# Kernel optimization log

Hardware: AMD Instinct MI355X
Metric: run time of the kernel (lower is better)

Reference implementation:

```python
import jax, jax.numpy as jnp
import numpy as np

N_NODES = 100000
N_EDGES = 1600000
S_FEAT = 16   # static node features
D_FEAT = 8    # dynamic node features
E_FEAT = 4    # edge features
K = 2
EDGE_IN = E_FEAT + 2 * S_FEAT + 2 * D_FEAT  # 52
HIDDEN = 2 * D_FEAT                          # 16


def setup_inputs() -> dict:
    key = jax.random.key(0)
    ks = jax.random.split(key, 12)
    inp = {
        "x_s": jax.random.normal(ks[0], (N_NODES, S_FEAT), jnp.float32),
        "x_d": jax.random.normal(ks[1], (N_NODES, D_FEAT), jnp.float32),
        "edge_attr": jax.random.normal(ks[2], (N_EDGES, E_FEAT), jnp.float32),
        # edge MLP: Linear(EDGE_IN->HIDDEN) + ReLU + Linear(HIDDEN->D_FEAT)
        "W1": jax.random.normal(ks[3], (HIDDEN, EDGE_IN), jnp.float32) / np.sqrt(EDGE_IN),
        "b1": jnp.zeros((HIDDEN,), jnp.float32),
        "W2": jax.random.normal(ks[4], (D_FEAT, HIDDEN), jnp.float32) / np.sqrt(HIDDEN),
        "b2": jnp.zeros((D_FEAT,), jnp.float32),
        # K+1 = 3 filter matrices, Linear(D->D, bias=False): y = x @ W.T
        "Wf0": jax.random.normal(ks[5], (D_FEAT, D_FEAT), jnp.float32) / np.sqrt(D_FEAT),
        "Wf1": jax.random.normal(ks[6], (D_FEAT, D_FEAT), jnp.float32) / np.sqrt(D_FEAT),
        "Wf2": jax.random.normal(ks[7], (D_FEAT, D_FEAT), jnp.float32) / np.sqrt(D_FEAT),
        "edge_index": jax.random.randint(ks[8], (2, N_EDGES), 0, N_NODES, jnp.int64
                                         if jax.config.jax_enable_x64 else jnp.int32),
    }
    return inp


def _edge_mlp(e, W1, b1, W2, b2):
    h = jax.nn.relu(e @ W1.T + b1)
    return h @ W2.T + b2


def reference(x_s, x_d, edge_attr, W1, b1, W2, b2, Wf0, Wf1, Wf2, edge_index):
    row, col = edge_index[0], edge_index[1]
    num_nodes = x_d.shape[0]

    # s_ij depends only on static inputs (x_s, x_d, edge_attr), not on `out`,
    # so it is identical across the K steps; compute it once. The per-step
    # boolean edge mask is applied multiplicatively below, which matches the
    # torch masked-gather/scatter exactly (normalization is per-edge).
    e_ij = jnp.concatenate(
        [x_s[row], x_s[col], x_d[row], x_d[col], edge_attr], axis=1)  # [E, 52]
    s_ij = _edge_mlp(e_ij, W1, b1, W2, b2)                            # [E, D]
    nrm = jnp.linalg.norm(s_ij, axis=1, keepdims=True)
    s_ij = jnp.where(nrm > 0, s_ij / jnp.where(nrm > 0, nrm, 1.0), 0.0)

    filters = [Wf0, Wf1, Wf2]
    out = x_d @ filters[0].T
    for k in range(K):
        mask = out.sum(1) != 0                         # [N]
        edge_mask = (mask[row] | mask[col]).astype(out.dtype)  # [E]
        hydraulic_gradient = out[col] - out[row]       # [E, D]
        shift_sum = hydraulic_gradient * s_ij * edge_mask[:, None]
        scattered = jax.ops.segment_sum(shift_sum, col, num_segments=num_nodes)
        scattered = scattered @ filters[k + 1].T
        out = out + scattered
    return out
```

## Files before the change

kernel.cpp:

```cpp
#include <hip/hip_runtime.h>
#include <hip/hip_fp16.h>

#define S_FEAT 16
#define D_FEAT 8
#define E_FEAT 4
#define EDGE_IN 52
#define HIDDEN 16
#define SCAN_CHUNK 2048
#define NSUB 8

typedef unsigned int uint4v __attribute__((ext_vector_type(4)));
typedef float float4v __attribute__((ext_vector_type(4)));
typedef int int2v __attribute__((ext_vector_type(2)));

__device__ __forceinline__ void mlp_sij(
    const float* __restrict__ x_s, const float* __restrict__ x_d,
    const float* __restrict__ edge_attr,
    const float* __restrict__ W1, const float* __restrict__ b1,
    const float* __restrict__ W2, const float* __restrict__ b2,
    int row, int col, int e, float s[D_FEAT])
{
    float in[EDGE_IN];
    {
        const float4* p = (const float4*)(x_s + (size_t)row * S_FEAT);
#pragma unroll
        for (int q = 0; q < 4; ++q) {
            float4 v = p[q];
            in[q * 4 + 0] = v.x; in[q * 4 + 1] = v.y;
            in[q * 4 + 2] = v.z; in[q * 4 + 3] = v.w;
        }
    }
    {
        const float4* p = (const float4*)(x_s + (size_t)col * S_FEAT);
#pragma unroll
        for (int q = 0; q < 4; ++q) {
            float4 v = p[q];
            in[16 + q * 4 + 0] = v.x; in[16 + q * 4 + 1] = v.y;
            in[16 + q * 4 + 2] = v.z; in[16 + q * 4 + 3] = v.w;
        }
    }
    {
        const float4* p = (const float4*)(x_d + (size_t)row * D_FEAT);
#pragma unroll
        for (int q = 0; q < 2; ++q) {
            float4 v = p[q];
            in[32 + q * 4 + 0] = v.x; in[32 + q * 4 + 1] = v.y;
            in[32 + q * 4 + 2] = v.z; in[32 + q * 4 + 3] = v.w;
        }
    }
    {
        const float4* p = (const float4*)(x_d + (size_t)col * D_FEAT);
#pragma unroll
        for (int q = 0; q < 2; ++q) {
            float4 v = p[q];
            in[40 + q * 4 + 0] = v.x; in[40 + q * 4 + 1] = v.y;
            in[40 + q * 4 + 2] = v.z; in[40 + q * 4 + 3] = v.w;
        }
    }
    {
        float4 v = *(const float4*)(edge_attr + (size_t)e * E_FEAT);
        in[48] = v.x; in[49] = v.y; in[50] = v.z; in[51] = v.w;
    }

    float h[HIDDEN];
#pragma unroll
    for (int i = 0; i < HIDDEN; ++i) {
        float acc = b1[i];
#pragma unroll
        for (int j = 0; j < EDGE_IN; ++j)
            acc = fmaf(in[j], W1[i * EDGE_IN + j], acc);
        h[i] = acc > 0.f ? acc : 0.f;
    }

    float nrm2 = 0.f;
#pragma unroll
    for (int i = 0; i < D_FEAT; ++i) {
        float acc = b2[i];
#pragma unroll
        for (int j = 0; j < HIDDEN; ++j)
            acc = fmaf(h[j], W2[i * HIDDEN + j], acc);
        s[i] = acc;
        nrm2 = fmaf(acc, acc, nrm2);
    }
    float nrm = sqrtf(nrm2);
    float inv = nrm > 0.f ? 1.f / nrm : 0.f;
#pragma unroll
    for (int i = 0; i < D_FEAT; ++i) s[i] *= inv;
}

__device__ __forceinline__ uint4v pack_rec(const float s[8], int row)
{
    int q[8];
#pragma unroll
    for (int i = 0; i < 8; ++i) {
        float v = fminf(fmaxf(s[i] * 2047.f, -2047.f), 2047.f);
        q[i] = (int)rintf(v) & 0xFFF;
    }
    uint4v r;
    r[0] = (unsigned)(q[0] | (q[1] << 12) | (q[2] << 24));
    r[1] = (unsigned)((q[2] >> 8) | (q[3] << 4) | (q[4] << 16) | (q[5] << 28));
    r[2] = (unsigned)((q[5] >> 4) | (q[6] << 8) | (q[7] << 20));
    r[3] = (unsigned)row;
    return r;
}

__device__ __forceinline__ float rec_s(uint4v r, int f)
{
    int off = f * 12;
    unsigned lo = off < 32 ? r[0] : (off < 64 ? r[1] : r[2]);
    unsigned hi = off < 32 ? r[1] : (off < 64 ? r[2] : 0u);
    unsigned sh = (unsigned)off & 31u;
    unsigned long long both = ((unsigned long long)hi << 32) | lo;
    int q = ((int)((unsigned)(both >> sh) << 20)) >> 20;
    return (float)q * (1.f / 2047.f);
}

__device__ __forceinline__ void unpack8h(uint4v w, float* dst)
{
#pragma unroll
    for (int i = 0; i < 4; ++i) {
        unsigned u = w[i];
        __half2 h = *reinterpret_cast<__half2*>(&u);
        float2 f = __half22float2(h);
        dst[2 * i] = f.x; dst[2 * i + 1] = f.y;
    }
}

__global__ __launch_bounds__(256) void zero_counts_kernel(int* __restrict__ counts, int M)
{
    int i = blockIdx.x * blockDim.x + threadIdx.x;
    if (i < M) counts[i] = 0;
}

__global__ __launch_bounds__(256) void hist_kernel(
    const int* __restrict__ ei, int E, int N, int* __restrict__ counts8)
{
    int e = blockIdx.x * blockDim.x + threadIdx.x;
    if (e >= E) return;
    int col = __builtin_nontemporal_load(ei + E + e);
    atomicAdd(&counts8[(threadIdx.x & (NSUB - 1)) * N + col], 1);
}

__global__ __launch_bounds__(256) void scan_local_kernel(
    const int* __restrict__ counts8, int* __restrict__ partial,
    int* __restrict__ blocksums, int N)
{
    __shared__ int sh[256];
    int b = blockIdx.x, t = threadIdx.x;
    int base = b * SCAN_CHUNK + t * 8;
    int v[8];
    int run = 0;
#pragma unroll
    for (int j = 0; j < 8; ++j) {
        int c = 0;
        if (base + j < N) {
#pragma unroll
            for (int s8 = 0; s8 < NSUB; ++s8)
                c += counts8[s8 * N + base + j];
        }
        v[j] = run;
        run += c;
    }
    sh[t] = run;
    __syncthreads();
#pragma unroll
    for (int st = 1; st < 256; st <<= 1) {
        int x = (t >= st) ? sh[t - st] : 0;
        __syncthreads();
        sh[t] += x;
        __syncthreads();
    }
    int excl = sh[t] - run;
    if (t == 255) blocksums[b] = sh[255];
#pragma unroll
    for (int j = 0; j < 8; ++j)
        if (base + j < N) partial[base + j] = excl + v[j];
}

__global__ __launch_bounds__(64) void scan_blk_kernel(int* __restrict__ bs, int NB)
{
    int lane = threadIdx.x;
    int carry = 0;
    for (int base = 0; base < NB; base += 64) {
        int i = base + lane;
        int orig = (i < NB) ? bs[i] : 0;
        int v = orig;
#pragma unroll
        for (int st = 1; st < 64; st <<= 1) {
            int t = __shfl_up(v, st);
            if (lane >= st) v += t;
        }
        if (i < NB) bs[i] = carry + v - orig;
        carry += __shfl(v, 63);
    }
}

__global__ __launch_bounds__(256) void scan_add_kernel(
    int* __restrict__ offsets, int* __restrict__ cursor,
    const int* __restrict__ blocksums, int N, int E)
{
    int i = blockIdx.x * blockDim.x + threadIdx.x;
    if (i < N) {
        int off = offsets[i] + blocksums[i / SCAN_CHUNK];
        offsets[i] = off;
        cursor[i]  = off;
    } else if (i == N) {
        offsets[N] = E;
    }
}

__global__ __launch_bounds__(256) void proj_scan_kernel(
    int* __restrict__ offsets, int* __restrict__ cursor,
    const int* __restrict__ blocksums,
    const float* __restrict__ x_s, const float* __restrict__ x_d,
    const float* __restrict__ W1, const float* __restrict__ b1,
    const float* __restrict__ Wf0,
    __half* __restrict__ PRh, __half* __restrict__ PCh,
    float* __restrict__ out, int N, int E)
{
    int n = blockIdx.x * blockDim.x + threadIdx.x;
    if (n > N) return;
    if (n == N) { offsets[N] = E; return; }
    {
        int off = offsets[n] + blocksums[n / SCAN_CHUNK];
        offsets[n] = off;
        cursor[n]  = off;
    }
    float xs[S_FEAT], xd[D_FEAT];
    {
        const float4* p = (const float4*)(x_s + (size_t)n * S_FEAT);
#pragma unroll
        for (int q = 0; q < 4; ++q) {
            float4 v = p[q];
            xs[q * 4 + 0] = v.x; xs[q * 4 + 1] = v.y;
            xs[q * 4 + 2] = v.z; xs[q * 4 + 3] = v.w;
        }
        const float4* pd = (const float4*)(x_d + (size_t)n * D_FEAT);
        float4 a = pd[0], b = pd[1];
        xd[0] = a.x; xd[1] = a.y; xd[2] = a.z; xd[3] = a.w;
        xd[4] = b.x; xd[5] = b.y; xd[6] = b.z; xd[7] = b.w;
    }
    __half prh[HIDDEN], pch[HIDDEN];
#pragma unroll
    for (int i = 0; i < HIDDEN; ++i) {
        const float* w = W1 + i * EDGE_IN;
        float a = b1[i], c = 0.f;
#pragma unroll
        for (int j = 0; j < S_FEAT; ++j) {
            a = fmaf(xs[j], w[j], a);
            c = fmaf(xs[j], w[16 + j], c);
        }
#pragma unroll
        for (int j = 0; j < D_FEAT; ++j) {
            a = fmaf(xd[j], w[32 + j], a);
            c = fmaf(xd[j], w[40 + j], c);
        }
        prh[i] = __float2half_rn(a);
        pch[i] = __float2half_rn(c);
    }
    {
        uint4v* pr = (uint4v*)(PRh + (size_t)n * HIDDEN);
        uint4v* pc = (uint4v*)(PCh + (size_t)n * HIDDEN);
        pr[0] = *(uint4v*)&prh[0]; pr[1] = *(uint4v*)&prh[8];
        pc[0] = *(uint4v*)&pch[0]; pc[1] = *(uint4v*)&pch[8];
    }
    float o[D_FEAT];
#pragma unroll
    for (int i = 0; i < D_FEAT; ++i) {
        float acc = 0.f;
#pragma unroll
        for (int j = 0; j < D_FEAT; ++j)
            acc = fmaf(xd[j], Wf0[i * D_FEAT + j], acc);
        o[i] = acc;
    }
    float4* op = (float4*)(out + (size_t)n * D_FEAT);
    op[0] = make_float4(o[0], o[1], o[2], o[3]);
    op[1] = make_float4(o[4], o[5], o[6], o[7]);
}

__device__ __forceinline__ void edge_work(
    const __half* __restrict__ PRh, const __half* __restrict__ PCh,
    const float* __restrict__ edge_attr,
    const float* __restrict__ W1,
    const float* __restrict__ W2, const float* __restrict__ b2,
    int row, int col, int e,
    int* __restrict__ cursor, uint4v* __restrict__ recs)
{
    float pr[HIDDEN], pc[HIDDEN];
    {
        const uint4v* p = (const uint4v*)(PRh + (size_t)row * HIDDEN);
        const uint4v* c = (const uint4v*)(PCh + (size_t)col * HIDDEN);
        uint4v p0 = p[0], p1 = p[1], c0 = c[0], c1 = c[1];
        unpack8h(p0, pr); unpack8h(p1, pr + 8);
        unpack8h(c0, pc); unpack8h(c1, pc + 8);
    }
    float4v ea = __builtin_nontemporal_load(
        (const float4v*)(edge_attr + (size_t)e * E_FEAT));

    float h[HIDDEN];
#pragma unroll
    for (int i = 0; i < HIDDEN; ++i) {
        const float* w = W1 + i * EDGE_IN + 48;
        float acc = pr[i] + pc[i];
        acc = fmaf(ea[0], w[0], acc);
        acc = fmaf(ea[1], w[1], acc);
        acc = fmaf(ea[2], w[2], acc);
        acc = fmaf(ea[3], w[3], acc);
        h[i] = acc > 0.f ? acc : 0.f;
    }

    float s[D_FEAT];
    float nrm2 = 0.f;
#pragma unroll
    for (int i = 0; i < D_FEAT; ++i) {
        float acc = b2[i];
#pragma unroll
        for (int j = 0; j < HIDDEN; ++j)
            acc = fmaf(h[j], W2[i * HIDDEN + j], acc);
        s[i] = acc;
        nrm2 = fmaf(acc, acc, nrm2);
    }
    float nrm = sqrtf(nrm2);
    float inv = nrm > 0.f ? 1.f / nrm : 0.f;
#pragma unroll
    for (int i = 0; i < D_FEAT; ++i) s[i] *= inv;

    uint4v rec = pack_rec(s, row);
    int pos = atomicAdd(&cursor[col], 1);
    __builtin_nontemporal_store(rec, recs + pos);
}

__global__ __launch_bounds__(256) void mlp_scatter_proj_kernel(
    const __half* __restrict__ PRh, const __half* __restrict__ PCh,
    const float* __restrict__ edge_attr,
    const float* __restrict__ W1,
    const float* __restrict__ W2, const float* __restrict__ b2,
    const int* __restrict__ ei, int E,
    int* __restrict__ cursor, uint4v* __restrict__ recs)
{
    int e0 = (blockIdx.x * blockDim.x + threadIdx.x) * 2;
    if (e0 >= E) return;
    if (e0 + 1 < E) {
        int2v rows = __builtin_nontemporal_load((const int2v*)(ei + e0));
        int2v cols = __builtin_nontemporal_load((const int2v*)(ei + E + e0));
        edge_work(PRh, PCh, edge_attr, W1, W2, b2, rows[0], cols[0], e0,     cursor, recs);
        edge_work(PRh, PCh, edge_attr, W1, W2, b2, rows[1], cols[1], e0 + 1, cursor, recs);
    } else {
        int row = ei[e0], col = ei[E + e0];
        edge_work(PRh, PCh, edge_attr, W1, W2, b2, row, col, e0, cursor, recs);
    }
}

__global__ __launch_bounds__(256) void mlp_scatter_direct_kernel(
    const float* __restrict__ x_s, const float* __restrict__ x_d,
    const float* __restrict__ edge_attr,
    const float* __restrict__ W1, const float* __restrict__ b1,
    const float* __restrict__ W2, const float* __restrict__ b2,
    const int* __restrict__ ei, int E,
    int* __restrict__ cursor, uint4v* __restrict__ recs)
{
    int e = blockIdx.x * blockDim.x + threadIdx.x;
    if (e >= E) return;
    int row = ei[e], col = ei[E + e];
    float s[D_FEAT];
    mlp_sij(x_s, x_d, edge_attr, W1, b1, W2, b2, row, col, e, s);
    uint4v rec = pack_rec(s, row);
    int pos = atomicAdd(&cursor[col], 1);
    __builtin_nontemporal_store(rec, recs + pos);
}

__global__ __launch_bounds__(256) void node_init_kernel(
    const float* __restrict__ x_d, const float* __restrict__ Wf0,
    float* __restrict__ out, int N)
{
    int n = blockIdx.x * blockDim.x + threadIdx.x;
    if (n >= N) return;
    float xd[D_FEAT];
    const float4* p = (const float4*)(x_d + (size_t)n * D_FEAT);
    float4 a = p[0], b = p[1];
    xd[0] = a.x; xd[1] = a.y; xd[2] = a.z; xd[3] = a.w;
    xd[4] = b.x; xd[5] = b.y; xd[6] = b.z; xd[7] = b.w;
    float o[D_FEAT];
#pragma unroll
    for (int i = 0; i < D_FEAT; ++i) {
        float acc = 0.f;
#pragma unroll
        for (int j = 0; j < D_FEAT; ++j)
            acc = fmaf(xd[j], Wf0[i * D_FEAT + j], acc);
        o[i] = acc;
    }
    float4* op = (float4*)(out + (size_t)n * D_FEAT);
    op[0] = make_float4(o[0], o[1], o[2], o[3]);
    op[1] = make_float4(o[4], o[5], o[6], o[7]);
}

__global__ __launch_bounds__(256) void csr_step_kernel(
    const float* __restrict__ out_in, float* __restrict__ out_out,
    const int* __restrict__ offsets, const uint4v* __restrict__ recs,
    const float* __restrict__ Wf, int N)
{
    int lane = threadIdx.x & 63;
    int node = blockIdx.x * 4 + (threadIdx.x >> 6);
    if (node >= N) return;
    int e_sub = lane >> 3, f = lane & 7;
    int beg = offsets[node], end = offsets[node + 1];
    float outc = out_in[(size_t)node * 8 + f];
    float sc = outc;
    sc += __shfl_xor(sc, 1); sc += __shfl_xor(sc, 2); sc += __shfl_xor(sc, 4);
    bool mc = (sc != 0.f);
    float acc = 0.f;
    for (int base = beg; base < end; base += 8) {
        int e = base + e_sub;
        bool valid = e < end;
        uint4v rec = (uint4v)(0u);
        if (valid) rec = __builtin_nontemporal_load(recs + e);
        int row = (int)rec[3];
        float s = rec_s(rec, f);
        float outr = out_in[(size_t)row * 8 + f];
        float sr = outr;
        sr += __shfl_xor(sr, 1); sr += __shfl_xor(sr, 2); sr += __shfl_xor(sr, 4);
        acc += (mc || sr != 0.f) ? (outc - outr) * s : 0.f;
    }
    acc += __shfl_xor(acc, 8);
    acc += __shfl_xor(acc, 16);
    acc += __shfl_xor(acc, 32);
    float upd = 0.f;
#pragma unroll
    for (int j = 0; j < 8; ++j) {
        float aj = __shfl(acc, (lane & ~7) | j);
        upd = fmaf(Wf[f * 8 + j], aj, upd);
    }
    if (e_sub == 0)
        out_out[(size_t)node * 8 + f] = outc + upd;
}

__global__ __launch_bounds__(256) void fb_node_init_kernel(
    const float* __restrict__ x_d, const float* __restrict__ Wf0,
    float* __restrict__ out, float* __restrict__ scattered, int N)
{
    int n = blockIdx.x * blockDim.x + threadIdx.x;
    if (n >= N) return;
    float xd[D_FEAT];
    const float4* p = (const float4*)(x_d + (size_t)n * D_FEAT);
    float4 a = p[0], b = p[1];
    xd[0] = a.x; xd[1] = a.y; xd[2] = a.z; xd[3] = a.w;
    xd[4] = b.x; xd[5] = b.y; xd[6] = b.z; xd[7] = b.w;
    float o[D_FEAT];
#pragma unroll
    for (int i = 0; i < D_FEAT; ++i) {
        float acc = 0.f;
#pragma unroll
        for (int j = 0; j < D_FEAT; ++j)
            acc = fmaf(xd[j], Wf0[i * D_FEAT + j], acc);
        o[i] = acc;
    }
    float4* op = (float4*)(out + (size_t)n * D_FEAT);
    op[0] = make_float4(o[0], o[1], o[2], o[3]);
    op[1] = make_float4(o[4], o[5], o[6], o[7]);
    float4* sp = (float4*)(scattered + (size_t)n * D_FEAT);
    sp[0] = make_float4(0.f, 0.f, 0.f, 0.f);
    sp[1] = make_float4(0.f, 0.f, 0.f, 0.f);
}

__global__ __launch_bounds__(256) void fb_edge_step_kernel(
    const float* __restrict__ x_s, const float* __restrict__ x_d,
    const float* __restrict__ edge_attr,
    const float* __restrict__ W1, const float* __restrict__ b1,
    const float* __restrict__ W2, const float* __restrict__ b2,
    const float* __restrict__ out,
    const int* __restrict__ ei, int E, float* __restrict__ scattered)
{
    int e = blockIdx.x * blockDim.x + threadIdx.x;
    if (e >= E) return;
    int row = ei[e], col = ei[E + e];
    const float4* pr = (const float4*)(out + (size_t)row * D_FEAT);
    const float4* pc = (const float4*)(out + (size_t)col * D_FEAT);
    float4 r0 = pr[0], r1 = pr[1], c0 = pc[0], c1 = pc[1];
    float srow = r0.x + r0.y + r0.z + r0.w + r1.x + r1.y + r1.z + r1.w;
    float scol = c0.x + c0.y + c0.z + c0.w + c1.x + c1.y + c1.z + c1.w;
    if (srow == 0.f && scol == 0.f) return;
    float s[D_FEAT];
    mlp_sij(x_s, x_d, edge_attr, W1, b1, W2, b2, row, col, e, s);
    float* dst = scattered + (size_t)col * D_FEAT;
    atomicAdd(dst + 0, (c0.x - r0.x) * s[0]);
    atomicAdd(dst + 1, (c0.y - r0.y) * s[1]);
    atomicAdd(dst + 2, (c0.z - r0.z) * s[2]);
    atomicAdd(dst + 3, (c0.w - r0.w) * s[3]);
    atomicAdd(dst + 4, (c1.x - r1.x) * s[4]);
    atomicAdd(dst + 5, (c1.y - r1.y) * s[5]);
    atomicAdd(dst + 6, (c1.z - r1.z) * s[6]);
    atomicAdd(dst + 7, (c1.w - r1.w) * s[7]);
}

__global__ __launch_bounds__(256) void fb_node_update_kernel(
    float* __restrict__ out, float* __restrict__ scattered,
    const float* __restrict__ Wf, int N)
{
    int n = blockIdx.x * blockDim.x + threadIdx.x;
    if (n >= N) return;
    float sc[D_FEAT];
    float4* sp = (float4*)(scattered + (size_t)n * D_FEAT);
    float4 a = sp[0], b = sp[1];
    sc[0] = a.x; sc[1] = a.y; sc[2] = a.z; sc[3] = a.w;
    sc[4] = b.x; sc[5] = b.y; sc[6] = b.z; sc[7] = b.w;
    sp[0] = make_float4(0.f, 0.f, 0.f, 0.f);
    sp[1] = make_float4(0.f, 0.f, 0.f, 0.f);
    float4* op = (float4*)(out + (size_t)n * D_FEAT);
    float4 o0 = op[0], o1 = op[1];
    float o[D_FEAT] = {o0.x, o0.y, o0.z, o0.w, o1.x, o1.y, o1.z, o1.w};
#pragma unroll
    for (int i = 0; i < D_FEAT; ++i) {
        float acc = 0.f;
#pragma unroll
        for (int j = 0; j < D_FEAT; ++j)
            acc = fmaf(sc[j], Wf[i * D_FEAT + j], acc);
        o[i] += acc;
    }
    op[0] = make_float4(o[0], o[1], o[2], o[3]);
    op[1] = make_float4(o[4], o[5], o[6], o[7]);
}

extern "C" void kernel_launch(void* const* d_in, const int* in_sizes, int n_in,
                              void* d_out, int out_size, void* d_ws, size_t ws_size,
                              hipStream_t stream) {
    const float* x_s       = (const float*)d_in[0];
    const float* x_d       = (const float*)d_in[1];
    const float* edge_attr = (const float*)d_in[2];
    const float* W1        = (const float*)d_in[3];
    const float* b1        = (const float*)d_in[4];
    const float* W2        = (const float*)d_in[5];
    const float* b2        = (const float*)d_in[6];
    const float* Wf[3]     = {(const float*)d_in[7], (const float*)d_in[8],
                              (const float*)d_in[9]};
    const int*   ei        = (const int*)d_in[10];

    const int N = in_sizes[1] / D_FEAT;
    const int E = in_sizes[10] / 2;

    float* out = (float*)d_out;

    size_t off = 0;
    auto carve = [&](size_t bytes) { size_t p = off; off = (off + bytes + 255) & ~255ULL; return p; };
    size_t o_counts  = carve((size_t)NSUB * N * 4);
    size_t o_offsets = carve((size_t)(N + 1) * 4);
    size_t o_cursor  = carve((size_t)(N + 1) * 4);
    size_t o_bsums   = carve(256 * 4);
    size_t o_bufA    = carve((size_t)N * D_FEAT * 4);
    size_t o_recs    = carve((size_t)E * 16);
    const size_t need_base = off;
    size_t o_PR      = carve((size_t)N * HIDDEN * 2);
    size_t o_PC      = carve((size_t)N * HIDDEN * 2);
    const size_t need_full = off;

    dim3 blk(256);
    dim3 gE((E + 255) / 256);
    dim3 gN((N + 255) / 256);

    if (ws_size >= need_base) {
        char* ws = (char*)d_ws;
        int*   counts8 = (int*)(ws + o_counts);
        int*   offsets = (int*)(ws + o_offsets);
        int*   cursor  = (int*)(ws + o_cursor);
        int*   bsums   = (int*)(ws + o_bsums);
        float* bufA    = (float*)(ws + o_bufA);
        uint4v* recs   = (uint4v*)(ws + o_recs);

        const int NB = (N + SCAN_CHUNK - 1) / SCAN_CHUNK;

        zero_counts_kernel<<<dim3((NSUB * N + 255) / 256), blk, 0, stream>>>(counts8, NSUB * N);
        hist_kernel<<<gE, blk, 0, stream>>>(ei, E, N, counts8);
        scan_local_kernel<<<dim3(NB), blk, 0, stream>>>(counts8, offsets, bsums, N);
        scan_blk_kernel<<<dim3(1), dim3(64), 0, stream>>>(bsums, NB);

        if (ws_size >= need_full) {
            __half* PRh = (__half*)(ws + o_PR);
            __half* PCh = (__half*)(ws + o_PC);
            proj_scan_kernel<<<dim3((N + 256) / 256), blk, 0, stream>>>(
                offsets, cursor, bsums, x_s, x_d, W1, b1, Wf[0],
                PRh, PCh, out, N, E);
            mlp_scatter_proj_kernel<<<dim3((E / 2 + 255) / 256), blk, 0, stream>>>(
                PRh, PCh, edge_attr, W1, W2, b2, ei, E, cursor, recs);
        } else {
            scan_add_kernel<<<dim3((N + 256) / 256), blk, 0, stream>>>(offsets, cursor, bsums, N, E);
            node_init_kernel<<<gN, blk, 0, stream>>>(x_d, Wf[0], out, N);
            mlp_scatter_direct_kernel<<<gE, blk, 0, stream>>>(
                x_s, x_d, edge_attr, W1, b1, W2, b2, ei, E, cursor, recs);
        }

        dim3 gC((N + 3) / 4);
        csr_step_kernel<<<gC, blk, 0, stream>>>(out, bufA, offsets, recs, Wf[1], N);
        csr_step_kernel<<<gC, blk, 0, stream>>>(bufA, out, offsets, recs, Wf[2], N);
    } else {
        float* scattered = (float*)d_ws;
        fb_node_init_kernel<<<gN, blk, 0, stream>>>(x_d, Wf[0], out, scattered, N);
        for (int k = 0; k < 2; ++k) {
            fb_edge_step_kernel<<<gE, blk, 0, stream>>>(
                x_s, x_d, edge_attr, W1, b1, W2, b2, out, ei, E, scattered);
            fb_node_update_kernel<<<gN, blk, 0, stream>>>(out, scattered, Wf[k + 1], N);
        }
    }
}
```

Baseline: 375.3 us.

## Fold block-sum scan into last scan block and replace zero kernel with memset

Removes the separate single-block scan kernel by having the last-finishing scan_local block, detected via an atomic done counter, perform the block-sum prefix scan. The zero-count kernel becomes a hipMemsetAsync that also clears the done counter. The edge MLP kernel now handles one edge per thread instead of two. This cuts launch count and serialization, at the cost of threadfence/atomic traffic and possibly less per-thread ILP in the edge kernel.

```diff
diff --git a/kernel.cpp b/kernel.cpp
--- a/kernel.cpp
+++ b/kernel.cpp
@@ -11,82 +11,6 @@
 
 typedef unsigned int uint4v __attribute__((ext_vector_type(4)));
 typedef float float4v __attribute__((ext_vector_type(4)));
-typedef int int2v __attribute__((ext_vector_type(2)));
-
-__device__ __forceinline__ void mlp_sij(
-    const float* __restrict__ x_s, const float* __restrict__ x_d,
-    const float* __restrict__ edge_attr,
-    const float* __restrict__ W1, const float* __restrict__ b1,
-    const float* __restrict__ W2, const float* __restrict__ b2,
-    int row, int col, int e, float s[D_FEAT])
-{
-    float in[EDGE_IN];
-    {
-        const float4* p = (const float4*)(x_s + (size_t)row * S_FEAT);
-#pragma unroll
-        for (int q = 0; q < 4; ++q) {
-            float4 v = p[q];
-            in[q * 4 + 0] = v.x; in[q * 4 + 1] = v.y;
-            in[q * 4 + 2] = v.z; in[q * 4 + 3] = v.w;
-        }
-    }
-    {
-        const float4* p = (const float4*)(x_s + (size_t)col * S_FEAT);
-#pragma unroll
-        for (int q = 0; q < 4; ++q) {
-            float4 v = p[q];
-            in[16 + q * 4 + 0] = v.x; in[16 + q * 4 + 1] = v.y;
-            in[16 + q * 4 + 2] = v.z; in[16 + q * 4 + 3] = v.w;
-        }
-    }
-    {
-        const float4* p = (const float4*)(x_d + (size_t)row * D_FEAT);
-#pragma unroll
-        for (int q = 0; q < 2; ++q) {
-            float4 v = p[q];
-            in[32 + q * 4 + 0] = v.x; in[32 + q * 4 + 1] = v.y;
-            in[32 + q * 4 + 2] = v.z; in[32 + q * 4 + 3] = v.w;
-        }
-    }
-    {
-        const float4* p = (const float4*)(x_d + (size_t)col * D_FEAT);
-#pragma unroll
-        for (int q = 0; q < 2; ++q) {
-            float4 v = p[q];
-            in[40 + q * 4 + 0] = v.x; in[40 + q * 4 + 1] = v.y;
-            in[40 + q * 4 + 2] = v.z; in[40 + q * 4 + 3] = v.w;
-        }
-    }
-    {
-        float4 v = *(const float4*)(edge_attr + (size_t)e * E_FEAT);
-        in[48] = v.x; in[49] = v.y; in[50] = v.z; in[51] = v.w;
-    }
-
-    float h[HIDDEN];
-#pragma unroll
-    for (int i = 0; i < HIDDEN; ++i) {
-        float acc = b1[i];
-#pragma unroll
-        for (int j = 0; j < EDGE_IN; ++j)
-            acc = fmaf(in[j], W1[i * EDGE_IN + j], acc);
-        h[i] = acc > 0.f ? acc : 0.f;
-    }
-
-    float nrm2 = 0.f;
-#pragma unroll
-    for (int i = 0; i < D_FEAT; ++i) {
-        float acc = b2[i];
-#pragma unroll
-        for (int j = 0; j < HIDDEN; ++j)
-            acc = fmaf(h[j], W2[i * HIDDEN + j], acc);
-        s[i] = acc;
-        nrm2 = fmaf(acc, acc, nrm2);
-    }
-    float nrm = sqrtf(nrm2);
-    float inv = nrm > 0.f ? 1.f / nrm : 0.f;
-#pragma unroll
-    for (int i = 0; i < D_FEAT; ++i) s[i] *= inv;
-}
 
 __device__ __forceinline__ uint4v pack_rec(const float s[8], int row)
 {
@@ -126,10 +50,114 @@
     }
 }
 
-__global__ __launch_bounds__(256) void zero_counts_kernel(int* __restrict__ counts, int M)
-{
-    int i = blockIdx.x * blockDim.x + threadIdx.x;
-    if (i < M) counts[i] = 0;
+__device__ __forceinline__ void proj_node(
+    int n, const float* __restrict__ x_s, const float* __restrict__ x_d,
+    const float* __restrict__ W1, const float* __restrict__ b1,
+    const float* __restrict__ Wf0,
+    __half* __restrict__ PRh, __half* __restrict__ PCh, float* __restrict__ out)
+{
+    float xs[S_FEAT], xd[D_FEAT];
+    {
+        const float4* p = (const float4*)(x_s + (size_t)n * S_FEAT);
+#pragma unroll
+        for (int q = 0; q < 4; ++q) {
+            float4 v = p[q];
+            xs[q * 4 + 0] = v.x; xs[q * 4 + 1] = v.y;
+            xs[q * 4 + 2] = v.z; xs[q * 4 + 3] = v.w;
+        }
+        const float4* pd = (const float4*)(x_d + (size_t)n * D_FEAT);
+        float4 a = pd[0], b = pd[1];
+        xd[0] = a.x; xd[1] = a.y; xd[2] = a.z; xd[3] = a.w;
+        xd[4] = b.x; xd[5] = b.y; xd[6] = b.z; xd[7] = b.w;
+    }
+    __half prh[HIDDEN], pch[HIDDEN];
+#pragma unroll
+    for (int i = 0; i < HIDDEN; ++i) {
+        const float* w = W1 + i * EDGE_IN;
+        float a = b1[i], c = 0.f;
+#pragma unroll
+        for (int j = 0; j < S_FEAT; ++j) {
+            a = fmaf(xs[j], w[j], a);
+            c = fmaf(xs[j], w[16 + j], c);
+        }
+#pragma unroll
+        for (int j = 0; j < D_FEAT; ++j) {
+            a = fmaf(xd[j], w[32 + j], a);
+            c = fmaf(xd[j], w[40 + j], c);
+        }
+        prh[i] = __float2half_rn(a);
+        pch[i] = __float2half_rn(c);
+    }
+    {
+        uint4v* pr = (uint4v*)(PRh + (size_t)n * HIDDEN);
+        uint4v* pc = (uint4v*)(PCh + (size_t)n * HIDDEN);
+        pr[0] = *(uint4v*)&prh[0]; pr[1] = *(uint4v*)&prh[8];
+        pc[0] = *(uint4v*)&pch[0]; pc[1] = *(uint4v*)&pch[8];
+    }
+    float o[D_FEAT];
+#pragma unroll
+    for (int i = 0; i < D_FEAT; ++i) {
+        float acc = 0.f;
+#pragma unroll
+        for (int j = 0; j < D_FEAT; ++j)
+            acc = fmaf(xd[j], Wf0[i * D_FEAT + j], acc);
+        o[i] = acc;
+    }
+    float4* op = (float4*)(out + (size_t)n * D_FEAT);
+    op[0] = make_float4(o[0], o[1], o[2], o[3]);
+    op[1] = make_float4(o[4], o[5], o[6], o[7]);
+}
+
+__device__ __forceinline__ void edge_work(
+    const __half* __restrict__ PRh, const __half* __restrict__ PCh,
+    const float* __restrict__ edge_attr,
+    const float* __restrict__ W1,
+    const float* __restrict__ W2, const float* __restrict__ b2,
+    int row, int col, int e,
+    int* __restrict__ cursor, uint4v* __restrict__ recs)
+{
+    float pr[HIDDEN], pc[HIDDEN];
+    {
+        const uint4v* p = (const uint4v*)(PRh + (size_t)row * HIDDEN);
+        const uint4v* c = (const uint4v*)(PCh + (size_t)col * HIDDEN);
+        uint4v p0 = p[0], p1 = p[1], c0 = c[0], c1 = c[1];
+        unpack8h(p0, pr); unpack8h(p1, pr + 8);
+        unpack8h(c0, pc); unpack8h(c1, pc + 8);
+    }
+    float4v ea = __builtin_nontemporal_load(
+        (const float4v*)(edge_attr + (size_t)e * E_FEAT));
+
+    float h[HIDDEN];
+#pragma unroll
+    for (int i = 0; i < HIDDEN; ++i) {
+        const float* w = W1 + i * EDGE_IN + 48;
+        float acc = pr[i] + pc[i];
+        acc = fmaf(ea[0], w[0], acc);
+        acc = fmaf(ea[1], w[1], acc);
+        acc = fmaf(ea[2], w[2], acc);
+        acc = fmaf(ea[3], w[3], acc);
+        h[i] = acc > 0.f ? acc : 0.f;
+    }
+
+    float s[D_FEAT];
+    float nrm2 = 0.f;
+#pragma unroll
+    for (int i = 0; i < D_FEAT; ++i) {
+        float acc = b2[i];
+#pragma unroll
+        for (int j = 0; j < HIDDEN; ++j)
+            acc = fmaf(h[j], W2[i * HIDDEN + j], acc);
+        s[i] = acc;
+        nrm2 = fmaf(acc, acc, nrm2);
+    }
+    float nrm = sqrtf(nrm2);
+    float inv = nrm > 0.f ? 1.f / nrm : 0.f;
+#pragma unroll
+    for (int i = 0; i < D_FEAT; ++i) s[i] *= inv;
+
+    uint4v rec = pack_rec(s, row);
+    int pos = atomicAdd(&cursor[col], 1);
+    __builtin_nontemporal_store(rec, recs + pos);
 }
 
 __global__ __launch_bounds__(256) void hist_kernel(
@@ -143,9 +171,10 @@
 
 __global__ __launch_bounds__(256) void scan_local_kernel(
     const int* __restrict__ counts8, int* __restrict__ partial,
-    int* __restrict__ blocksums, int N)
+    int* __restrict__ bsums, int* __restrict__ done, int N, int NB)
 {
     __shared__ int sh[256];
+    __shared__ int amLast;
     int b = blockIdx.x, t = threadIdx.x;
     int base = b * SCAN_CHUNK + t * 8;
     int v[8];
@@ -171,41 +200,29 @@
         __syncthreads();
     }
     int excl = sh[t] - run;
-    if (t == 255) blocksums[b] = sh[255];
 #pragma unroll
     for (int j = 0; j < 8; ++j)
         if (base + j < N) partial[base + j] = excl + v[j];
-}
-
-__global__ __launch_bounds__(64) void scan_blk_kernel(int* __restrict__ bs, int NB)
-{
-    int lane = threadIdx.x;
-    int carry = 0;
-    for (int base = 0; base < NB; base += 64) {
-        int i = base + lane;
-        int orig = (i < NB) ? bs[i] : 0;
-        int v = orig;
-#pragma unroll
-        for (int st = 1; st < 64; st <<= 1) {
-            int t = __shfl_up(v, st);
-            if (lane >= st) v += t;
-        }
-        if (i < NB) bs[i] = carry + v - orig;
-        carry += __shfl(v, 63);
-    }
-}
-
-__global__ __launch_bounds__(256) void scan_add_kernel(
-    int* __restrict__ offsets, int* __restrict__ cursor,
-    const int* __restrict__ blocksums, int N, int E)
-{
-    int i = blockIdx.x * blockDim.x + threadIdx.x;
-    if (i < N) {
-        int off = offsets[i] + blocksums[i / SCAN_CHUNK];
-        offsets[i] = off;
-        cursor[i]  = off;
-    } else if (i == N) {
-        offsets[N] = E;
+
+    if (t == 255) atomicExch(&bsums[b], sh[255]);
+    __threadfence();
+    if (t == 0) amLast = (atomicAdd(done, 1) == NB - 1);
+    __syncthreads();
+    if (amLast && t < 64) {
+        int lane = t;
+        int carry = 0;
+        for (int cb = 0; cb < NB; cb += 64) {
+            int i = cb + lane;
+            int orig = (i < NB) ? atomicAdd(&bsums[i], 0) : 0;
+            int x = orig;
+#pragma unroll
+            for (int st = 1; st < 64; st <<= 1) {
+                int y = __shfl_up(x, st);
+                if (lane >= st) x += y;
+            }
+            if (i < NB) atomicExch(&bsums[i], carry + x - orig);
+            carry += __shfl(x, 63);
+        }
     }
 }
 
@@ -221,113 +238,10 @@
     int n = blockIdx.x * blockDim.x + threadIdx.x;
     if (n > N) return;
     if (n == N) { offsets[N] = E; return; }
-    {
-        int off = offsets[n] + blocksums[n / SCAN_CHUNK];
-        offsets[n] = off;
-        cursor[n]  = off;
-    }
-    float xs[S_FEAT], xd[D_FEAT];
-    {
-        const float4* p = (const float4*)(x_s + (size_t)n * S_FEAT);
-#pragma unroll
-        for (int q = 0; q < 4; ++q) {
-            float4 v = p[q];
-            xs[q * 4 + 0] = v.x; xs[q * 4 + 1] = v.y;
-            xs[q * 4 + 2] = v.z; xs[q * 4 + 3] = v.w;
-        }
-        const float4* pd = (const float4*)(x_d + (size_t)n * D_FEAT);
-        float4 a = pd[0], b = pd[1];
-        xd[0] = a.x; xd[1] = a.y; xd[2] = a.z; xd[3] = a.w;
-        xd[4] = b.x; xd[5] = b.y; xd[6] = b.z; xd[7] = b.w;
-    }
-    __half prh[HIDDEN], pch[HIDDEN];
-#pragma unroll
-    for (int i = 0; i < HIDDEN; ++i) {
-        const float* w = W1 + i * EDGE_IN;
-        float a = b1[i], c = 0.f;
-#pragma unroll
-        for (int j = 0; j < S_FEAT; ++j) {
-            a = fmaf(xs[j], w[j], a);
-            c = fmaf(xs[j], w[16 + j], c);
-        }
-#pragma unroll
-        for (int j = 0; j < D_FEAT; ++j) {
-            a = fmaf(xd[j], w[32 + j], a);
-            c = fmaf(xd[j], w[40 + j], c);
-        }
-        prh[i] = __float2half_rn(a);
-        pch[i] = __float2half_rn(c);
-    }
-    {
-        uint4v* pr = (uint4v*)(PRh + (size_t)n * HIDDEN);
-        uint4v* pc = (uint4v*)(PCh + (size_t)n * HIDDEN);
-        pr[0] = *(uint4v*)&prh[0]; pr[1] = *(uint4v*)&prh[8];
-        pc[0] = *(uint4v*)&pch[0]; pc[1] = *(uint4v*)&pch[8];
-    }
-    float o[D_FEAT];
-#pragma unroll
-    for (int i = 0; i < D_FEAT; ++i) {
-        float acc = 0.f;
-#pragma unroll
-        for (int j = 0; j < D_FEAT; ++j)
-            acc = fmaf(xd[j], Wf0[i * D_FEAT + j], acc);
-        o[i] = acc;
-    }
-    float4* op = (float4*)(out + (size_t)n * D_FEAT);
-    op[0] = make_float4(o[0], o[1], o[2], o[3]);
-    op[1] = make_float4(o[4], o[5], o[6], o[7]);
-}
-
-__device__ __forceinline__ void edge_work(
-    const __half* __restrict__ PRh, const __half* __restrict__ PCh,
-    const float* __restrict__ edge_attr,
-    const float* __restrict__ W1,
-    const float* __restrict__ W2, const float* __restrict__ b2,
-    int row, int col, int e,
-    int* __restrict__ cursor, uint4v* __restrict__ recs)
-{
-    float pr[HIDDEN], pc[HIDDEN];
-    {
-        const uint4v* p = (const uint4v*)(PRh + (size_t)row * HIDDEN);
-        const uint4v* c = (const uint4v*)(PCh + (size_t)col * HIDDEN);
-        uint4v p0 = p[0], p1 = p[1], c0 = c[0], c1 = c[1];
-        unpack8h(p0, pr); unpack8h(p1, pr + 8);
-        unpack8h(c0, pc); unpack8h(c1, pc + 8);
-    }
-    float4v ea = __builtin_nontemporal_load(
-        (const float4v*)(edge_attr + (size_t)e * E_FEAT));
-
-    float h[HIDDEN];
-#pragma unroll
-    for (int i = 0; i < HIDDEN; ++i) {
-        const float* w = W1 + i * EDGE_IN + 48;
-        float acc = pr[i] + pc[i];
-        acc = fmaf(ea[0], w[0], acc);
-        acc = fmaf(ea[1], w[1], acc);
-        acc = fmaf(ea[2], w[2], acc);
-        acc = fmaf(ea[3], w[3], acc);
-        h[i] = acc > 0.f ? acc : 0.f;
-    }
-
-    float s[D_FEAT];
-    float nrm2 = 0.f;
-#pragma unroll
-    for (int i = 0; i < D_FEAT; ++i) {
-        float acc = b2[i];
-#pragma unroll
-        for (int j = 0; j < HIDDEN; ++j)
-            acc = fmaf(h[j], W2[i * HIDDEN + j], acc);
-        s[i] = acc;
-        nrm2 = fmaf(acc, acc, nrm2);
-    }
-    float nrm = sqrtf(nrm2);
-    float inv = nrm > 0.f ? 1.f / nrm : 0.f;
-#pragma unroll
-    for (int i = 0; i < D_FEAT; ++i) s[i] *= inv;
-
-    uint4v rec = pack_rec(s, row);
-    int pos = atomicAdd(&cursor[col], 1);
-    __builtin_nontemporal_store(rec, recs + pos);
+    int off2 = offsets[n] + blocksums[n / SCAN_CHUNK];
+    offsets[n] = off2;
+    cursor[n]  = off2;
+    proj_node(n, x_s, x_d, W1, b1, Wf0, PRh, PCh, out);
 }
 
 __global__ __launch_bounds__(256) void mlp_scatter_proj_kernel(
@@ -338,60 +252,11 @@
     const int* __restrict__ ei, int E,
     int* __restrict__ cursor, uint4v* __restrict__ recs)
 {
-    int e0 = (blockIdx.x * blockDim.x + threadIdx.x) * 2;
-    if (e0 >= E) return;
-    if (e0 + 1 < E) {
-        int2v rows = __builtin_nontemporal_load((const int2v*)(ei + e0));
-        int2v cols = __builtin_nontemporal_load((const int2v*)(ei + E + e0));
-        edge_work(PRh, PCh, edge_attr, W1, W2, b2, rows[0], cols[0], e0,     cursor, recs);
-        edge_work(PRh, PCh, edge_attr, W1, W2, b2, rows[1], cols[1], e0 + 1, cursor, recs);
-    } else {
-        int row = ei[e0], col = ei[E + e0];
-        edge_work(PRh, PCh, edge_attr, W1, W2, b2, row, col, e0, cursor, recs);
-    }
-}
-
-__global__ __launch_bounds__(256) void mlp_scatter_direct_kernel(
-    const float* __restrict__ x_s, const float* __restrict__ x_d,
-    const float* __restrict__ edge_attr,
-    const float* __restrict__ W1, const float* __restrict__ b1,
-    const float* __restrict__ W2, const float* __restrict__ b2,
-    const int* __restrict__ ei, int E,
-    int* __restrict__ cursor, uint4v* __restrict__ recs)
-{
     int e = blockIdx.x * blockDim.x + threadIdx.x;
     if (e >= E) return;
-    int row = ei[e], col = ei[E + e];
-    float s[D_FEAT];
-    mlp_sij(x_s, x_d, edge_attr, W1, b1, W2, b2, row, col, e, s);
-    uint4v rec = pack_rec(s, row);
-    int pos = atomicAdd(&cursor[col], 1);
-    __builtin_nontemporal_store(rec, recs + pos);
-}
-
-__global__ __launch_bounds__(256) void node_init_kernel(
-    const float* __restrict__ x_d, const float* __restrict__ Wf0,
-    float* __restrict__ out, int N)
-{
-    int n = blockIdx.x * blockDim.x + threadIdx.x;
-    if (n >= N) return;
-    float xd[D_FEAT];
-    const float4* p = (const float4*)(x_d + (size_t)n * D_FEAT);
-    float4 a = p[0], b = p[1];
-    xd[0] = a.x; xd[1] = a.y; xd[2] = a.z; xd[3] = a.w;
-    xd[4] = b.x; xd[5] = b.y; xd[6] = b.z; xd[7] = b.w;
-    float o[D_FEAT];
-#pragma unroll
-    for (int i = 0; i < D_FEAT; ++i) {
-        float acc = 0.f;
-#pragma unroll
-        for (int j = 0; j < D_FEAT; ++j)
-            acc = fmaf(xd[j], Wf0[i * D_FEAT + j], acc);
-        o[i] = acc;
-    }
-    float4* op = (float4*)(out + (size_t)n * D_FEAT);
-    op[0] = make_float4(o[0], o[1], o[2], o[3]);
-    op[1] = make_float4(o[4], o[5], o[6], o[7]);
+    int row = __builtin_nontemporal_load(ei + e);
+    int col = __builtin_nontemporal_load(ei + E + e);
+    edge_work(PRh, PCh, edge_attr, W1, W2, b2, row, col, e, cursor, recs);
 }
 
 __global__ __launch_bounds__(256) void csr_step_kernel(
@@ -434,6 +299,136 @@
         out_out[(size_t)node * 8 + f] = outc + upd;
 }
 
+__device__ __forceinline__ void mlp_sij(
+    const float* __restrict__ x_s, const float* __restrict__ x_d,
+    const float* __restrict__ edge_attr,
+    const float* __restrict__ W1, const float* __restrict__ b1,
+    const float* __restrict__ W2, const float* __restrict__ b2,
+    int row, int col, int e, float s[D_FEAT])
+{
+    float in[EDGE_IN];
+    {
+        const float4* p = (const float4*)(x_s + (size_t)row * S_FEAT);
+#pragma unroll
+        for (int q = 0; q < 4; ++q) {
+            float4 v = p[q];
+            in[q * 4 + 0] = v.x; in[q * 4 + 1] = v.y;
+            in[q * 4 + 2] = v.z; in[q * 4 + 3] = v.w;
+        }
+    }
+    {
+        const float4* p = (const float4*)(x_s + (size_t)col * S_FEAT);
+#pragma unroll
+        for (int q = 0; q < 4; ++q) {
+            float4 v = p[q];
+            in[16 + q * 4 + 0] = v.x; in[16 + q * 4 + 1] = v.y;
+            in[16 + q * 4 + 2] = v.z; in[16 + q * 4 + 3] = v.w;
+        }
+    }
+    {
+        const float4* p = (const float4*)(x_d + (size_t)row * D_FEAT);
+#pragma unroll
+        for (int q = 0; q < 2; ++q) {
+            float4 v = p[q];
+            in[32 + q * 4 + 0] = v.x; in[32 + q * 4 + 1] = v.y;
+            in[32 + q * 4 + 2] = v.z; in[32 + q * 4 + 3] = v.w;
+        }
+    }
+    {
+        const float4* p = (const float4*)(x_d + (size_t)col * D_FEAT);
+#pragma unroll
+        for (int q = 0; q < 2; ++q) {
+            float4 v = p[q];
+            in[40 + q * 4 + 0] = v.x; in[40 + q * 4 + 1] = v.y;
+            in[40 + q * 4 + 2] = v.z; in[40 + q * 4 + 3] = v.w;
+        }
+    }
+    {
+        float4 v = *(const float4*)(edge_attr + (size_t)e * E_FEAT);
+        in[48] = v.x; in[49] = v.y; in[50] = v.z; in[51] = v.w;
+    }
+    float h[HIDDEN];
+#pragma unroll
+    for (int i = 0; i < HIDDEN; ++i) {
+        float acc = b1[i];
+#pragma unroll
+        for (int j = 0; j < EDGE_IN; ++j)
+            acc = fmaf(in[j], W1[i * EDGE_IN + j], acc);
+        h[i] = acc > 0.f ? acc : 0.f;
+    }
+    float nrm2 = 0.f;
+#pragma unroll
+    for (int i = 0; i < D_FEAT; ++i) {
+        float acc = b2[i];
+#pragma unroll
+        for (int j = 0; j < HIDDEN; ++j)
+            acc = fmaf(h[j], W2[i * HIDDEN + j], acc);
+        s[i] = acc;
+        nrm2 = fmaf(acc, acc, nrm2);
+    }
+    float nrm = sqrtf(nrm2);
+    float inv = nrm > 0.f ? 1.f / nrm : 0.f;
+#pragma unroll
+    for (int i = 0; i < D_FEAT; ++i) s[i] *= inv;
+}
+
+__global__ __launch_bounds__(256) void scan_add_kernel(
+    int* __restrict__ offsets, int* __restrict__ cursor,
+    const int* __restrict__ blocksums, int N, int E)
+{
+    int i = blockIdx.x * blockDim.x + threadIdx.x;
+    if (i < N) {
+        int off2 = offsets[i] + blocksums[i / SCAN_CHUNK];
+        offsets[i] = off2;
+        cursor[i]  = off2;
+    } else if (i == N) {
+        offsets[N] = E;
+    }
+}
+
+__global__ __launch_bounds__(256) void node_init_kernel(
+    const float* __restrict__ x_d, const float* __restrict__ Wf0,
+    float* __restrict__ out, int N)
+{
+    int n = blockIdx.x * blockDim.x + threadIdx.x;
+    if (n >= N) return;
+    float xd[D_FEAT];
+    const float4* p = (const float4*)(x_d + (size_t)n * D_FEAT);
+    float4 a = p[0], b = p[1];
+    xd[0] = a.x; xd[1] = a.y; xd[2] = a.z; xd[3] = a.w;
+    xd[4] = b.x; xd[5] = b.y; xd[6] = b.z; xd[7] = b.w;
+    float o[D_FEAT];
+#pragma unroll
+    for (int i = 0; i < D_FEAT; ++i) {
+        float acc = 0.f;
+#pragma unroll
+        for (int j = 0; j < D_FEAT; ++j)
+            acc = fmaf(xd[j], Wf0[i * D_FEAT + j], acc);
+        o[i] = acc;
+    }
+    float4* op = (float4*)(out + (size_t)n * D_FEAT);
+    op[0] = make_float4(o[0], o[1], o[2], o[3]);
+    op[1] = make_float4(o[4], o[5], o[6], o[7]);
+}
+
+__global__ __launch_bounds__(256) void mlp_scatter_direct_kernel(
+    const float* __restrict__ x_s, const float* __restrict__ x_d,
+    const float* __restrict__ edge_attr,
+    const float* __restrict__ W1, const float* __restrict__ b1,
+    const float* __restrict__ W2, const float* __restrict__ b2,
+    const int* __restrict__ ei, int E,
+    int* __restrict__ cursor, uint4v* __restrict__ recs)
+{
+    int e = blockIdx.x * blockDim.x + threadIdx.x;
+    if (e >= E) return;
+    int row = ei[e], col = ei[E + e];
+    float s[D_FEAT];
+    mlp_sij(x_s, x_d, edge_attr, W1, b1, W2, b2, row, col, e, s);
+    uint4v rec = pack_rec(s, row);
+    int pos = atomicAdd(&cursor[col], 1);
+    __builtin_nontemporal_store(rec, recs + pos);
+}
+
 __global__ __launch_bounds__(256) void fb_node_init_kernel(
     const float* __restrict__ x_d, const float* __restrict__ Wf0,
     float* __restrict__ out, float* __restrict__ scattered, int N)
@@ -530,18 +525,21 @@
     const float* b1        = (const float*)d_in[4];
     const float* W2        = (const float*)d_in[5];
     const float* b2        = (const float*)d_in[6];
-    const float* Wf[3]     = {(const float*)d_in[7], (const float*)d_in[8],
-                              (const float*)d_in[9]};
+    const float* Wf0       = (const float*)d_in[7];
+    const float* Wf1       = (const float*)d_in[8];
+    const float* Wf2       = (const float*)d_in[9];
     const int*   ei        = (const int*)d_in[10];
 
-    const int N = in_sizes[1] / D_FEAT;
-    const int E = in_sizes[10] / 2;
+    int N = in_sizes[1] / D_FEAT;
+    int E = in_sizes[10] / 2;
 
     float* out = (float*)d_out;
 
     size_t off = 0;
     auto carve = [&](size_t bytes) { size_t p = off; off = (off + bytes + 255) & ~255ULL; return p; };
     size_t o_counts  = carve((size_t)NSUB * N * 4);
+    size_t o_done    = carve(4);
+    const size_t zero_len = off;
     size_t o_offsets = carve((size_t)(N + 1) * 4);
     size_t o_cursor  = carve((size_t)(N + 1) * 4);
     size_t o_bsums   = carve(256 * 4);
@@ -559,6 +557,7 @@
     if (ws_size >= need_base) {
         char* ws = (char*)d_ws;
         int*   counts8 = (int*)(ws + o_counts);
+        int*   done    = (int*)(ws + o_done);
         int*   offsets = (int*)(ws + o_offsets);
         int*   cursor  = (int*)(ws + o_cursor);
         int*   bsums   = (int*)(ws + o_bsums);
@@ -567,36 +566,37 @@
 
         const int NB = (N + SCAN_CHUNK - 1) / SCAN_CHUNK;
 
-        zero_counts_kernel<<<dim3((NSUB * N + 255) / 256), blk, 0, stream>>>(counts8, NSUB * N);
+        hipMemsetAsync(ws, 0, zero_len, stream);
         hist_kernel<<<gE, blk, 0, stream>>>(ei, E, N, counts8);
-        scan_local_kernel<<<dim3(NB), blk, 0, stream>>>(counts8, offsets, bsums, N);
-        scan_blk_kernel<<<dim3(1), dim3(64), 0, stream>>>(bsums, NB);
+        scan_local_kernel<<<dim3(NB), blk, 0, stream>>>(
+            counts8, offsets, bsums, done, N, NB);
 
         if (ws_size >= need_full) {
             __half* PRh = (__half*)(ws + o_PR);
             __half* PCh = (__half*)(ws + o_PC);
             proj_scan_kernel<<<dim3((N + 256) / 256), blk, 0, stream>>>(
-                offsets, cursor, bsums, x_s, x_d, W1, b1, Wf[0],
-                PRh, PCh, out, N, E);
-            mlp_scatter_proj_kernel<<<dim3((E / 2 + 255) / 256), blk, 0, stream>>>(
+                offsets, cursor, bsums, x_s, x_d, W1, b1, Wf0, PRh, PCh, out, N, E);
+            mlp_scatter_proj_kernel<<<gE, blk, 0, stream>>>(
                 PRh, PCh, edge_attr, W1, W2, b2, ei, E, cursor, recs);
         } else {
-            scan_add_kernel<<<dim3((N + 256) / 256), blk, 0, stream>>>(offsets, cursor, bsums, N, E);
-            node_init_kernel<<<gN, blk, 0, stream>>>(x_d, Wf[0], out, N);
+            scan_add_kernel<<<dim3((N + 256) / 256), blk, 0, stream>>>(
+                offsets, cursor, bsums, N, E);
+            node_init_kernel<<<gN, blk, 0, stream>>>(x_d, Wf0, out, N);
             mlp_scatter_direct_kernel<<<gE, blk, 0, stream>>>(
                 x_s, x_d, edge_attr, W1, b1, W2, b2, ei, E, cursor, recs);
         }
 
         dim3 gC((N + 3) / 4);
-        csr_step_kernel<<<gC, blk, 0, stream>>>(out, bufA, offsets, recs, Wf[1], N);
-        csr_step_kernel<<<gC, blk, 0, stream>>>(bufA, out, offsets, recs, Wf[2], N);
+        csr_step_kernel<<<gC, blk, 0, stream>>>(out, bufA, offsets, recs, Wf1, N);
+        csr_step_kernel<<<gC, blk, 0, stream>>>(bufA, out, offsets, recs, Wf2, N);
     } else {
         float* scattered = (float*)d_ws;
-        fb_node_init_kernel<<<gN, blk, 0, stream>>>(x_d, Wf[0], out, scattered, N);
+        fb_node_init_kernel<<<gN, blk, 0, stream>>>(x_d, Wf0, out, scattered, N);
         for (int k = 0; k < 2; ++k) {
+            const float* Wfk = (k == 0) ? Wf1 : Wf2;
             fb_edge_step_kernel<<<gE, blk, 0, stream>>>(
                 x_s, x_d, edge_attr, W1, b1, W2, b2, out, ei, E, scattered);
-            fb_node_update_kernel<<<gN, blk, 0, stream>>>(out, scattered, Wf[k + 1], N);
-        }
-    }
-}
+            fb_node_update_kernel<<<gN, blk, 0, stream>>>(out, scattered, Wfk, N);
+        }
+    }
+}
```

Result: no change. 372.8 us (-0.7%).
